# Kernel optimization log

Hardware: AMD Instinct MI355X
Metric: run time of the kernel (lower is better)

## Reference

```python
import jax, jax.numpy as jnp
import numpy as np

B, T, C = 4, 2048, 1024
N_HEAD = 16
HEAD_DIM = C // N_HEAD

def setup_inputs() -> dict:
    key = jax.random.key(0)
    k1, k2, k3, k4, k5 = jax.random.split(key, 5)
    sigma = (1.0 / C) ** 0.5  # encoder_var=1 default
    return {
        "x": jax.random.normal(k1, (B, T, C), dtype=jnp.float32),
        "W_attn": jax.random.normal(k2, (3 * C, C), dtype=jnp.float32) * sigma,
        "b_attn": jax.random.normal(k3, (3 * C,), dtype=jnp.float32),
        "W_proj": jax.random.normal(k4, (C, C), dtype=jnp.float32) * sigma,
        "b_proj": jax.random.normal(k5, (C,), dtype=jnp.float32),
    }

def reference(x, W_attn, b_attn, W_proj, b_proj):
    Bq, Tq, Cq = x.shape
    qkv = x @ W_attn.T + b_attn              # [B,T,3C]
    q, k, v = jnp.split(qkv, 3, axis=-1)
    def to_heads(t):
        return t.reshape(Bq, Tq, N_HEAD, HEAD_DIM).transpose(0, 2, 1, 3)  # [B,H,T,D]
    q, k, v = to_heads(q), to_heads(k), to_heads(v)
    # NOTE: original scales by 1/head_dim (not 1/sqrt(head_dim))
    att = jnp.einsum('bhqd,bhkd->bhqk', q, k) * (1.0 / HEAD_DIM)
    causal = jnp.tril(jnp.ones((Tq, Tq), dtype=bool))
    att = jnp.where(causal[None, None], att, -jnp.inf)
    att = jax.nn.softmax(att, axis=-1)
    y = jnp.einsum('bhqk,bhkd->bhqd', att, v)
    y = y.transpose(0, 2, 1, 3).reshape(Bq, Tq, Cq)
    return y @ W_proj.T + b_proj
```

## Files before the change

### kernel.cpp

```cpp
#include <hip/hip_runtime.h>

typedef __attribute__((ext_vector_type(8))) short s16x8;
typedef __attribute__((ext_vector_type(4))) float f32x4;
typedef __attribute__((ext_vector_type(4))) unsigned short u16x4;

#define T_  2048
#define C_  1024
#define D_  64

__device__ __forceinline__ unsigned short f2bf(float f){
  union { float fv; unsigned int u; } v; v.fv = f;
  unsigned int r = v.u + 0x7FFFu + ((v.u >> 16) & 1u);
  return (unsigned short)(r >> 16);
}

__device__ __forceinline__ float exp2_asm(float x){
  float r; asm("v_exp_f32 %0, %1" : "=v"(r) : "v"(x)); return r;
}
__device__ __forceinline__ unsigned int cvtpk(float lo, float hi){
  unsigned int r; asm("v_cvt_pk_bf16_f32 %0, %1, %2" : "=v"(r) : "v"(lo), "v"(hi)); return r;
}

__device__ __forceinline__ void gload_lds16(const void* g, void* l){
  __builtin_amdgcn_global_load_lds(
      (const __attribute__((address_space(1))) unsigned int*)g,
      (__attribute__((address_space(3))) unsigned int*)l, 16, 0, 0);
}

__global__ __launch_bounds__(256) void cvt_kernel(const float* __restrict__ src,
                                                  unsigned short* __restrict__ dst){
  size_t i = ((size_t)blockIdx.x * 256u + threadIdx.x) * 8u;
  f32x4 a = *(const f32x4*)(src + i);
  f32x4 b = *(const f32x4*)(src + i + 4);
  s16x8 o;
  #pragma unroll
  for (int j = 0; j < 4; ++j){ o[j] = (short)f2bf(a[j]); o[4+j] = (short)f2bf(b[j]); }
  *(s16x8*)(dst + i) = o;
}

template<int MODE>
__global__ __launch_bounds__(256) void gemm_bt(
    const unsigned short* __restrict__ A, const unsigned short* __restrict__ Bw,
    const float* __restrict__ bias, int M, int N, int K,
    unsigned short* __restrict__ q_ws, unsigned short* __restrict__ k_ws,
    unsigned short* __restrict__ vT_ws, float* __restrict__ out)
{
  __shared__ unsigned short As[2][128*32];
  __shared__ unsigned short Bs[2][128*32];
  const int tid = threadIdx.x;
  const int lane = tid & 63, wid = tid >> 6;
  const int g = lane >> 4, lr = lane & 15;
  const int m0 = blockIdx.y * 128, n0 = blockIdx.x * 128;
  const int wr = wid >> 1, wc = wid & 1;

  f32x4 acc[4][4];
  #pragma unroll
  for (int i = 0; i < 4; ++i)
    #pragma unroll
    for (int j = 0; j < 4; ++j) acc[i][j] = (f32x4){0.f,0.f,0.f,0.f};

  auto stage = [&](int kt, int buf){
    const int k0 = kt << 5;
    #pragma unroll
    for (int j = 0; j < 2; ++j){
      const int c = wid*128 + j*64 + lane;
      const int row = c >> 2, kc = c & 3;
      gload_lds16((const char*)A  + (((size_t)(m0+row))*K + k0)*2 + kc*16,
                  (char*)&As[buf][0] + (size_t)c*16);
      gload_lds16((const char*)Bw + (((size_t)(n0+row))*K + k0)*2 + kc*16,
                  (char*)&Bs[buf][0] + (size_t)c*16);
    }
  };

  const int nk = K >> 5;
  stage(0, 0);
  __syncthreads();

  for (int kt = 0; kt < nk; ++kt){
    const int cur = kt & 1;
    if (kt + 1 < nk) stage(kt + 1, cur ^ 1);
    s16x8 af[4], bf[4];
    #pragma unroll
    for (int i = 0; i < 4; ++i)
      af[i] = *(const s16x8*)&As[cur][(wr*64 + i*16 + lr)*32 + g*8];
    #pragma unroll
    for (int j = 0; j < 4; ++j)
      bf[j] = *(const s16x8*)&Bs[cur][(wc*64 + j*16 + lr)*32 + g*8];
    #pragma unroll
    for (int i = 0; i < 4; ++i)
      #pragma unroll
      for (int j = 0; j < 4; ++j)
        acc[i][j] = __builtin_amdgcn_mfma_f32_16x16x32_bf16(af[i], bf[j], acc[i][j], 0, 0, 0);
    __syncthreads();
  }

  #pragma unroll
  for (int i = 0; i < 4; ++i){
    #pragma unroll
    for (int j = 0; j < 4; ++j){
      const int n = n0 + wc*64 + j*16 + lr;
      const float bv = bias[n];
      #pragma unroll
      for (int r = 0; r < 4; ++r){
        const int m = m0 + wr*64 + i*16 + g*4 + r;
        const float val = acc[i][j][r] + bv;
        if (MODE == 0){
          const int which = n >> 10;
          const int cc = n & 1023;
          const int h = cc >> 6, d = cc & 63;
          const int bq = m >> 11, t = m & 2047;
          const int bh = bq*16 + h;
          if (which == 0)      q_ws[((size_t)bh*T_ + t)*D_ + d] = f2bf(val * 0.022542110013890054f);
          else if (which == 1) k_ws[((size_t)bh*T_ + t)*D_ + d] = f2bf(val);
          else                 vT_ws[((size_t)bh*D_ + d)*T_ + t] = f2bf(val);
        } else {
          out[(size_t)m*N + n] = val;
        }
      }
    }
  }
}

__global__ __launch_bounds__(256, 4) void attn_kernel(
    const unsigned short* __restrict__ q_ws, const unsigned short* __restrict__ k_ws,
    const unsigned short* __restrict__ vT_ws, unsigned short* __restrict__ y_ws)
{
  __shared__ __align__(16) unsigned short Ks[2][64*64];
  __shared__ __align__(16) unsigned short Vs[2][64*64];

  const int tid = threadIdx.x;
  const int lane = tid & 63, wid = tid >> 6;
  const int g = lane >> 4, lr = lane & 15;
  const int orig = (int)blockIdx.x;
  const int wgid = (orig & 7) * 128 + (orig >> 3);
  const int p  = wgid & 15;
  const int bh = wgid >> 4;
  const int qwA = p*64 + wid*16,  qwB = (31 - p)*64 + wid*16;
  const int qrowA = qwA + lr,     qrowB = qwB + lr;
  const int swz = (lr & 7) << 4;

  const unsigned short* Qb = q_ws  + (size_t)bh*T_*D_;
  const unsigned short* Kb = k_ws  + (size_t)bh*T_*D_;
  const unsigned short* Vb = vT_ws + (size_t)bh*D_*T_;

  auto stage = [&](int t, int buf){
    const int kt0 = t << 6;
    #pragma unroll
    for (int s = 0; s < 2; ++s){
      const int c = s*256 + tid;
      const int r = c >> 3;
      const int scol = ((c & 7) << 4) ^ ((r & 7) << 4);
      gload_lds16((const char*)Kb + ((size_t)(kt0 + r)*D_)*2 + scol,
                  (char*)&Ks[buf][0] + c*16);
      gload_lds16((const char*)Vb + ((size_t)r*T_ + kt0)*2 + scol,
                  (char*)&Vs[buf][0] + c*16);
    }
  };

  const s16x8 bqA0 = *(const s16x8*)&Qb[(size_t)(qwA+lr)*D_ + g*8];
  const s16x8 bqA1 = *(const s16x8*)&Qb[(size_t)(qwA+lr)*D_ + 32 + g*8];
  const s16x8 bqB0 = *(const s16x8*)&Qb[(size_t)(qwB+lr)*D_ + g*8];
  const s16x8 bqB1 = *(const s16x8*)&Qb[(size_t)(qwB+lr)*D_ + 32 + g*8];

  s16x8 ones;
  #pragma unroll
  for (int j = 0; j < 8; ++j) ones[j] = (short)0x3F80;

  f32x4 yA[4], yB[4];
  #pragma unroll
  for (int dt = 0; dt < 4; ++dt){ yA[dt] = (f32x4){0.f,0.f,0.f,0.f}; yB[dt] = (f32x4){0.f,0.f,0.f,0.f}; }
  f32x4 lacA = (f32x4){0.f,0.f,0.f,0.f}, lacB = (f32x4){0.f,0.f,0.f,0.f};
  float mA = -1e30f, mB = -1e30f;

  const int ntA = p + 1, ntB = 32 - p;
  stage(0, 0);
  __syncthreads();

  for (int t = 0; t < ntB; ++t){
    const int cur = t & 1;
    if (t + 1 < ntB) stage(t + 1, cur ^ 1);
    const int kt0 = t << 6;
    const unsigned short* Kt = &Ks[cur][0];
    const unsigned short* Vt = &Vs[cur][0];
    unsigned short* Pw = &Ks[cur][wid*1024];
    const bool actA = (t < ntA);

    f32x4 sB[4], sA[4];
    #pragma unroll
    for (int kk = 0; kk < 4; ++kk){
      const int row = kk*16 + lr;
      const s16x8 a0 = *(const s16x8*)&Kt[row*64 + (((g*16)      ^ swz) >> 1)];
      const s16x8 a1 = *(const s16x8*)&Kt[row*64 + (((64 + g*16) ^ swz) >> 1)];
      f32x4 acc = (f32x4){0.f,0.f,0.f,0.f};
      acc = __builtin_amdgcn_mfma_f32_16x16x32_bf16(a0, bqB0, acc, 0, 0, 0);
      acc = __builtin_amdgcn_mfma_f32_16x16x32_bf16(a1, bqB1, acc, 0, 0, 0);
      sB[kk] = acc;
      if (actA){
        f32x4 acc2 = (f32x4){0.f,0.f,0.f,0.f};
        acc2 = __builtin_amdgcn_mfma_f32_16x16x32_bf16(a0, bqA0, acc2, 0, 0, 0);
        acc2 = __builtin_amdgcn_mfma_f32_16x16x32_bf16(a1, bqA1, acc2, 0, 0, 0);
        sA[kk] = acc2;
      }
    }

    if (kt0 + 63 > qwB){
      #pragma unroll
      for (int kk = 0; kk < 4; ++kk)
        #pragma unroll
        for (int r = 0; r < 4; ++r)
          if (kt0 + kk*16 + g*4 + r > qrowB) sB[kk][r] = -1e30f;
    }
    {
      float m01 = fmaxf(fmaxf(sB[0][0], sB[0][1]), fmaxf(sB[0][2], sB[0][3]));
      float m23 = fmaxf(fmaxf(sB[1][0], sB[1][1]), fmaxf(sB[1][2], sB[1][3]));
      float m45 = fmaxf(fmaxf(sB[2][0], sB[2][1]), fmaxf(sB[2][2], sB[2][3]));
      float m67 = fmaxf(fmaxf(sB[3][0], sB[3][1]), fmaxf(sB[3][2], sB[3][3]));
      float mx = fmaxf(fmaxf(m01, m23), fmaxf(m45, m67));
      mx = fmaxf(mx, __shfl_xor(mx, 16, 64));
      mx = fmaxf(mx, __shfl_xor(mx, 32, 64));
      if (!__all(mx <= mB + 8.f)){
        const float mnew = fmaxf(mB, mx);
        const float corr = exp2_asm(mB - mnew);
        mB = mnew;
        lacB[0] *= corr;
        #pragma unroll
        for (int dt = 0; dt < 4; ++dt)
          #pragma unroll
          for (int r = 0; r < 4; ++r) yB[dt][r] *= corr;
      }
    }
    union { unsigned int u[2]; u16x4 v; } pkB[4];
    #pragma unroll
    for (int kk = 0; kk < 4; ++kk){
      const float e0 = exp2_asm(sB[kk][0] - mB);
      const float e1 = exp2_asm(sB[kk][1] - mB);
      const float e2 = exp2_asm(sB[kk][2] - mB);
      const float e3 = exp2_asm(sB[kk][3] - mB);
      pkB[kk].u[0] = cvtpk(e0, e1);
      pkB[kk].u[1] = cvtpk(e2, e3);
    }

    asm volatile("s_barrier" ::: "memory");

    #pragma unroll
    for (int kk = 0; kk < 4; ++kk)
      *(u16x4*)&Pw[lr*64 + (((kk*32 + g*8) ^ swz) >> 1)] = pkB[kk].v;
    asm volatile("" ::: "memory");
    {
      const s16x8 p0 = *(const s16x8*)&Pw[lr*64 + (((g*16)      ^ swz) >> 1)];
      const s16x8 p1 = *(const s16x8*)&Pw[lr*64 + (((64 + g*16) ^ swz) >> 1)];
      lacB = __builtin_amdgcn_mfma_f32_16x16x32_bf16(ones, p0, lacB, 0, 0, 0);
      lacB = __builtin_amdgcn_mfma_f32_16x16x32_bf16(ones, p1, lacB, 0, 0, 0);
      #pragma unroll
      for (int dt = 0; dt < 4; ++dt){
        const int vrow = dt*16 + lr;
        const s16x8 v0 = *(const s16x8*)&Vt[vrow*64 + (((g*16)      ^ swz) >> 1)];
        const s16x8 v1 = *(const s16x8*)&Vt[vrow*64 + (((64 + g*16) ^ swz) >> 1)];
        yB[dt] = __builtin_amdgcn_mfma_f32_16x16x32_bf16(v0, p0, yB[dt], 0, 0, 0);
        yB[dt] = __builtin_amdgcn_mfma_f32_16x16x32_bf16(v1, p1, yB[dt], 0, 0, 0);
      }
    }

    if (actA){
      if (kt0 + 63 > qwA){
        #pragma unroll
        for (int kk = 0; kk < 4; ++kk)
          #pragma unroll
          for (int r = 0; r < 4; ++r)
            if (kt0 + kk*16 + g*4 + r > qrowA) sA[kk][r] = -1e30f;
      }
      float m01 = fmaxf(fmaxf(sA[0][0], sA[0][1]), fmaxf(sA[0][2], sA[0][3]));
      float m23 = fmaxf(fmaxf(sA[1][0], sA[1][1]), fmaxf(sA[1][2], sA[1][3]));
      float m45 = fmaxf(fmaxf(sA[2][0], sA[2][1]), fmaxf(sA[2][2], sA[2][3]));
      float m67 = fmaxf(fmaxf(sA[3][0], sA[3][1]), fmaxf(sA[3][2], sA[3][3]));
      float mx = fmaxf(fmaxf(m01, m23), fmaxf(m45, m67));
      mx = fmaxf(mx, __shfl_xor(mx, 16, 64));
      mx = fmaxf(mx, __shfl_xor(mx, 32, 64));
      if (!__all(mx <= mA + 8.f)){
        const float mnew = fmaxf(mA, mx);
        const float corr = exp2_asm(mA - mnew);
        mA = mnew;
        lacA[0] *= corr;
        #pragma unroll
        for (int dt = 0; dt < 4; ++dt)
          #pragma unroll
          for (int r = 0; r < 4; ++r) yA[dt][r] *= corr;
      }
      union { unsigned int u[2]; u16x4 v; } pkA[4];
      #pragma unroll
      for (int kk = 0; kk < 4; ++kk){
        const float e0 = exp2_asm(sA[kk][0] - mA);
        const float e1 = exp2_asm(sA[kk][1] - mA);
        const float e2 = exp2_asm(sA[kk][2] - mA);
        const float e3 = exp2_asm(sA[kk][3] - mA);
        pkA[kk].u[0] = cvtpk(e0, e1);
        pkA[kk].u[1] = cvtpk(e2, e3);
      }
      asm volatile("" ::: "memory");
      #pragma unroll
      for (int kk = 0; kk < 4; ++kk)
        *(u16x4*)&Pw[lr*64 + (((kk*32 + g*8) ^ swz) >> 1)] = pkA[kk].v;
      asm volatile("" ::: "memory");
      const s16x8 p0 = *(const s16x8*)&Pw[lr*64 + (((g*16)      ^ swz) >> 1)];
      const s16x8 p1 = *(const s16x8*)&Pw[lr*64 + (((64 + g*16) ^ swz) >> 1)];
      lacA = __builtin_amdgcn_mfma_f32_16x16x32_bf16(ones, p0, lacA, 0, 0, 0);
      lacA = __builtin_amdgcn_mfma_f32_16x16x32_bf16(ones, p1, lacA, 0, 0, 0);
      #pragma unroll
      for (int dt = 0; dt < 4; ++dt){
        const int vrow = dt*16 + lr;
        const s16x8 v0 = *(const s16x8*)&Vt[vrow*64 + (((g*16)      ^ swz) >> 1)];
        const s16x8 v1 = *(const s16x8*)&Vt[vrow*64 + (((64 + g*16) ^ swz) >> 1)];
        yA[dt] = __builtin_amdgcn_mfma_f32_16x16x32_bf16(v0, p0, yA[dt], 0, 0, 0);
        yA[dt] = __builtin_amdgcn_mfma_f32_16x16x32_bf16(v1, p1, yA[dt], 0, 0, 0);
      }
    }

    __syncthreads();
  }

  const int bq = bh >> 4, h = bh & 15;
  {
    const float inv = 1.f / lacB[0];
    #pragma unroll
    for (int dt = 0; dt < 4; ++dt){
      union { unsigned int u[2]; u16x4 v; } w;
      w.u[0] = cvtpk(yB[dt][0]*inv, yB[dt][1]*inv);
      w.u[1] = cvtpk(yB[dt][2]*inv, yB[dt][3]*inv);
      *(u16x4*)&y_ws[((size_t)(bq*T_ + qwB + lr))*C_ + h*64 + dt*16 + g*4] = w.v;
    }
  }
  {
    const float inv = 1.f / lacA[0];
    #pragma unroll
    for (int dt = 0; dt < 4; ++dt){
      union { unsigned int u[2]; u16x4 v; } w;
      w.u[0] = cvtpk(yA[dt][0]*inv, yA[dt][1]*inv);
      w.u[1] = cvtpk(yA[dt][2]*inv, yA[dt][3]*inv);
      *(u16x4*)&y_ws[((size_t)(bq*T_ + qwA + lr))*C_ + h*64 + dt*16 + g*4] = w.v;
    }
  }
}

extern "C" void kernel_launch(void* const* d_in, const int* in_sizes, int n_in,
                              void* d_out, int out_size, void* d_ws, size_t ws_size,
                              hipStream_t stream) {
  const float* x  = (const float*)d_in[0];
  const float* Wa = (const float*)d_in[1];
  const float* ba = (const float*)d_in[2];
  const float* Wp = (const float*)d_in[3];
  const float* bp = (const float*)d_in[4];
  float* out = (float*)d_out;

  char* ws = (char*)d_ws;
  const size_t MB = 1024u*1024u;
  unsigned short* xb  = (unsigned short*)(ws + 0);
  unsigned short* wab = (unsigned short*)(ws + 16*MB);
  unsigned short* wpb = (unsigned short*)(ws + 22*MB);
  unsigned short* qws = (unsigned short*)(ws + 24*MB);
  unsigned short* kws = (unsigned short*)(ws + 40*MB);
  unsigned short* vT  = (unsigned short*)(ws + 56*MB);
  unsigned short* yws = (unsigned short*)(ws + 72*MB);

  cvt_kernel<<<4096, 256, 0, stream>>>(x,  xb);
  cvt_kernel<<<1536, 256, 0, stream>>>(Wa, wab);
  cvt_kernel<<< 512, 256, 0, stream>>>(Wp, wpb);

  gemm_bt<0><<<dim3(24, 64), 256, 0, stream>>>(xb, wab, ba, 8192, 3072, 1024,
                                               qws, kws, vT, nullptr);
  attn_kernel<<<dim3(1024), 256, 0, stream>>>(qws, kws, vT, yws);
  gemm_bt<1><<<dim3(8, 64), 256, 0, stream>>>(yws, wpb, bp, 8192, 1024, 1024,
                                              nullptr, nullptr, nullptr, out);
}
```

Measured before the change: 207.7 us.

## Retile GEMMs to 256x128x64 with swizzled LDS, deeper prefetch and XCD remap

The projection GEMM kernel moves to 512-thread blocks computing 256x128 tiles with a K-step of 64. It uses XOR-swizzled LDS layouts to avoid bank conflicts and keeps two stages in flight via vmcnt-based waits instead of full syncthreads. Block IDs are remapped across the 8 XCDs for L2 locality, and MFMA sections run at raised priority. The aim is more operand reuse per LDS load and better overlap of global loads with compute. The cost is higher LDS use (96KB per block) and register pressure, which reduce occupancy.

```diff
diff --git a/kernel.cpp b/kernel.cpp
--- a/kernel.cpp
+++ b/kernel.cpp
@@ -39,71 +39,123 @@
 }
 
 template<int MODE>
-__global__ __launch_bounds__(256) void gemm_bt(
+__global__ __launch_bounds__(512, 2) void gemm_bt(
     const unsigned short* __restrict__ A, const unsigned short* __restrict__ Bw,
-    const float* __restrict__ bias, int M, int N, int K,
+    const float* __restrict__ bias, int M, int N, int K, int nbx,
     unsigned short* __restrict__ q_ws, unsigned short* __restrict__ k_ws,
     unsigned short* __restrict__ vT_ws, float* __restrict__ out)
 {
-  __shared__ unsigned short As[2][128*32];
-  __shared__ unsigned short Bs[2][128*32];
+  __shared__ unsigned short Asm[2][256*64];
+  __shared__ unsigned short Bsm[2][128*64];
   const int tid = threadIdx.x;
   const int lane = tid & 63, wid = tid >> 6;
   const int g = lane >> 4, lr = lane & 15;
-  const int m0 = blockIdx.y * 128, n0 = blockIdx.x * 128;
-  const int wr = wid >> 1, wc = wid & 1;
-
-  f32x4 acc[4][4];
+  const int wm = wid >> 2, wn = wid & 3;
+  const int nwg = (int)gridDim.x;
+  const int cpx = nwg >> 3;
+  const int orig = (int)blockIdx.x;
+  const int wgid = (orig & 7) * cpx + (orig >> 3);
+  const int bx = wgid % nbx, by = wgid / nbx;
+  const int m0 = by * 256, n0 = bx * 128;
+  const int swz = (lr & 7) << 4;
+
+  f32x4 acc[8][2];
   #pragma unroll
-  for (int i = 0; i < 4; ++i)
-    #pragma unroll
-    for (int j = 0; j < 4; ++j) acc[i][j] = (f32x4){0.f,0.f,0.f,0.f};
+  for (int i = 0; i < 8; ++i){ acc[i][0] = (f32x4){0.f,0.f,0.f,0.f}; acc[i][1] = (f32x4){0.f,0.f,0.f,0.f}; }
 
   auto stage = [&](int kt, int buf){
-    const int k0 = kt << 5;
+    const int k0 = kt << 6;
+    #pragma unroll
+    for (int j = 0; j < 4; ++j){
+      const int c = j*512 + tid;
+      const int row = c >> 3, jc = (c & 7) << 4;
+      gload_lds16((const char*)A + ((size_t)(m0+row)*K + k0)*2 + (jc ^ ((row & 7) << 4)),
+                  (char*)&Asm[buf][0] + (size_t)c*16);
+    }
     #pragma unroll
     for (int j = 0; j < 2; ++j){
-      const int c = wid*128 + j*64 + lane;
-      const int row = c >> 2, kc = c & 3;
-      gload_lds16((const char*)A  + (((size_t)(m0+row))*K + k0)*2 + kc*16,
-                  (char*)&As[buf][0] + (size_t)c*16);
-      gload_lds16((const char*)Bw + (((size_t)(n0+row))*K + k0)*2 + kc*16,
-                  (char*)&Bs[buf][0] + (size_t)c*16);
+      const int c = j*512 + tid;
+      const int row = c >> 3, jc = (c & 7) << 4;
+      gload_lds16((const char*)Bw + ((size_t)(n0+row)*K + k0)*2 + (jc ^ ((row & 7) << 4)),
+                  (char*)&Bsm[buf][0] + (size_t)c*16);
     }
   };
 
-  const int nk = K >> 5;
+  const int nk = K >> 6;
   stage(0, 0);
-  __syncthreads();
+  stage(1, 1);
 
   for (int kt = 0; kt < nk; ++kt){
     const int cur = kt & 1;
-    if (kt + 1 < nk) stage(kt + 1, cur ^ 1);
-    s16x8 af[4], bf[4];
-    #pragma unroll
-    for (int i = 0; i < 4; ++i)
-      af[i] = *(const s16x8*)&As[cur][(wr*64 + i*16 + lr)*32 + g*8];
-    #pragma unroll
-    for (int j = 0; j < 4; ++j)
-      bf[j] = *(const s16x8*)&Bs[cur][(wc*64 + j*16 + lr)*32 + g*8];
-    #pragma unroll
-    for (int i = 0; i < 4; ++i)
-      #pragma unroll
-      for (int j = 0; j < 4; ++j)
-        acc[i][j] = __builtin_amdgcn_mfma_f32_16x16x32_bf16(af[i], bf[j], acc[i][j], 0, 0, 0);
-    __syncthreads();
+    if (kt < nk - 1) asm volatile("s_waitcnt vmcnt(6)" ::: "memory");
+    else             asm volatile("s_waitcnt vmcnt(0)" ::: "memory");
+    asm volatile("s_barrier" ::: "memory");
+
+    const char* At = (const char*)&Asm[cur][0];
+    const char* Bt = (const char*)&Bsm[cur][0];
+
+    s16x8 bf[2][2];
+    #pragma unroll
+    for (int ni = 0; ni < 2; ++ni){
+      const int row = wn*32 + ni*16 + lr;
+      #pragma unroll
+      for (int s = 0; s < 2; ++s)
+        bf[ni][s] = *(const s16x8*)(Bt + row*128 + ((s*64 + g*16) ^ swz));
+    }
+
+    {
+      s16x8 af[4][2];
+      #pragma unroll
+      for (int mi = 0; mi < 4; ++mi){
+        const int row = wm*128 + mi*16 + lr;
+        #pragma unroll
+        for (int s = 0; s < 2; ++s)
+          af[mi][s] = *(const s16x8*)(At + row*128 + ((s*64 + g*16) ^ swz));
+      }
+      __builtin_amdgcn_s_setprio(1);
+      #pragma unroll
+      for (int mi = 0; mi < 4; ++mi)
+        #pragma unroll
+        for (int ni = 0; ni < 2; ++ni){
+          acc[mi][ni] = __builtin_amdgcn_mfma_f32_16x16x32_bf16(af[mi][0], bf[ni][0], acc[mi][ni], 0, 0, 0);
+          acc[mi][ni] = __builtin_amdgcn_mfma_f32_16x16x32_bf16(af[mi][1], bf[ni][1], acc[mi][ni], 0, 0, 0);
+        }
+      __builtin_amdgcn_s_setprio(0);
+    }
+    {
+      s16x8 af[4][2];
+      #pragma unroll
+      for (int mi = 0; mi < 4; ++mi){
+        const int row = wm*128 + (mi+4)*16 + lr;
+        #pragma unroll
+        for (int s = 0; s < 2; ++s)
+          af[mi][s] = *(const s16x8*)(At + row*128 + ((s*64 + g*16) ^ swz));
+      }
+      __builtin_amdgcn_s_setprio(1);
+      #pragma unroll
+      for (int mi = 0; mi < 4; ++mi)
+        #pragma unroll
+        for (int ni = 0; ni < 2; ++ni){
+          acc[mi+4][ni] = __builtin_amdgcn_mfma_f32_16x16x32_bf16(af[mi][0], bf[ni][0], acc[mi+4][ni], 0, 0, 0);
+          acc[mi+4][ni] = __builtin_amdgcn_mfma_f32_16x16x32_bf16(af[mi][1], bf[ni][1], acc[mi+4][ni], 0, 0, 0);
+        }
+      __builtin_amdgcn_s_setprio(0);
+    }
+
+    asm volatile("s_barrier" ::: "memory");
+    if (kt + 2 < nk) stage(kt + 2, cur);
   }
 
   #pragma unroll
-  for (int i = 0; i < 4; ++i){
-    #pragma unroll
-    for (int j = 0; j < 4; ++j){
-      const int n = n0 + wc*64 + j*16 + lr;
+  for (int mi = 0; mi < 8; ++mi){
+    #pragma unroll
+    for (int ni = 0; ni < 2; ++ni){
+      const int n = n0 + wn*32 + ni*16 + lr;
       const float bv = bias[n];
       #pragma unroll
       for (int r = 0; r < 4; ++r){
-        const int m = m0 + wr*64 + i*16 + g*4 + r;
-        const float val = acc[i][j][r] + bv;
+        const int m = m0 + wm*128 + mi*16 + g*4 + r;
+        const float val = acc[mi][ni][r] + bv;
         if (MODE == 0){
           const int which = n >> 10;
           const int cc = n & 1023;
@@ -365,9 +417,9 @@
   cvt_kernel<<<1536, 256, 0, stream>>>(Wa, wab);
   cvt_kernel<<< 512, 256, 0, stream>>>(Wp, wpb);
 
-  gemm_bt<0><<<dim3(24, 64), 256, 0, stream>>>(xb, wab, ba, 8192, 3072, 1024,
-                                               qws, kws, vT, nullptr);
+  gemm_bt<0><<<dim3(768), 512, 0, stream>>>(xb, wab, ba, 8192, 3072, 1024, 24,
+                                            qws, kws, vT, nullptr);
   attn_kernel<<<dim3(1024), 256, 0, stream>>>(qws, kws, vT, yws);
-  gemm_bt<1><<<dim3(8, 64), 256, 0, stream>>>(yws, wpb, bp, 8192, 1024, 1024,
-                                              nullptr, nullptr, nullptr, out);
-}
+  gemm_bt<1><<<dim3(256), 512, 0, stream>>>(yws, wpb, bp, 8192, 1024, 1024, 8,
+                                            nullptr, nullptr, nullptr, out);
+}
```

New measurement: 204.3 us. Within noise of the previous version (-1.6%).

## Restructure GEMM with BK=64, XOR-swizzled LDS, vmcnt pipelining and XCD-aware block remap

Applied to the files above, without the earlier changes.

The GEMM kernels now load 64-wide K tiles into an XOR-swizzled LDS layout to avoid bank conflicts. Two stages are kept in flight, waited on with explicit vmcnt counts and raw barriers instead of __syncthreads. Blocks are remapped across the eight XCDs for better L2 locality, and MFMA sections get raised wave priority. The cost is twice the LDS (64KB per block) and a hand-written wait/barrier protocol that must stay correct.

```diff
diff --git a/kernel.cpp b/kernel.cpp
--- a/kernel.cpp
+++ b/kernel.cpp
@@ -39,19 +39,25 @@
 }
 
 template<int MODE>
-__global__ __launch_bounds__(256) void gemm_bt(
+__global__ __launch_bounds__(256, 2) void gemm_bt(
     const unsigned short* __restrict__ A, const unsigned short* __restrict__ Bw,
-    const float* __restrict__ bias, int M, int N, int K,
+    const float* __restrict__ bias, int M, int N, int K, int nbx,
     unsigned short* __restrict__ q_ws, unsigned short* __restrict__ k_ws,
     unsigned short* __restrict__ vT_ws, float* __restrict__ out)
 {
-  __shared__ unsigned short As[2][128*32];
-  __shared__ unsigned short Bs[2][128*32];
+  __shared__ unsigned short Asm[2][128*64];
+  __shared__ unsigned short Bsm[2][128*64];
   const int tid = threadIdx.x;
   const int lane = tid & 63, wid = tid >> 6;
   const int g = lane >> 4, lr = lane & 15;
-  const int m0 = blockIdx.y * 128, n0 = blockIdx.x * 128;
   const int wr = wid >> 1, wc = wid & 1;
+  const int nwg = (int)gridDim.x;
+  const int cpx = nwg >> 3;
+  const int orig = (int)blockIdx.x;
+  const int wgid = (orig & 7) * cpx + (orig >> 3);
+  const int bx = wgid % nbx, by = wgid / nbx;
+  const int m0 = by * 128, n0 = bx * 128;
+  const int swz = (lr & 7) << 4;
 
   f32x4 acc[4][4];
   #pragma unroll
@@ -60,50 +66,68 @@
     for (int j = 0; j < 4; ++j) acc[i][j] = (f32x4){0.f,0.f,0.f,0.f};
 
   auto stage = [&](int kt, int buf){
-    const int k0 = kt << 5;
-    #pragma unroll
-    for (int j = 0; j < 2; ++j){
-      const int c = wid*128 + j*64 + lane;
-      const int row = c >> 2, kc = c & 3;
-      gload_lds16((const char*)A  + (((size_t)(m0+row))*K + k0)*2 + kc*16,
-                  (char*)&As[buf][0] + (size_t)c*16);
-      gload_lds16((const char*)Bw + (((size_t)(n0+row))*K + k0)*2 + kc*16,
-                  (char*)&Bs[buf][0] + (size_t)c*16);
+    const int k0 = kt << 6;
+    #pragma unroll
+    for (int j = 0; j < 4; ++j){
+      const int c = j*256 + tid;
+      const int row = c >> 3, jc = c & 7;
+      const int sc = (jc ^ (row & 7)) << 4;
+      gload_lds16((const char*)A  + ((size_t)(m0+row)*K + k0)*2 + sc,
+                  (char*)&Asm[buf][0] + (size_t)c*16);
+      gload_lds16((const char*)Bw + ((size_t)(n0+row)*K + k0)*2 + sc,
+                  (char*)&Bsm[buf][0] + (size_t)c*16);
     }
   };
 
-  const int nk = K >> 5;
+  const int nk = K >> 6;
   stage(0, 0);
-  __syncthreads();
-
-  for (int kt = 0; kt < nk; ++kt){
-    const int cur = kt & 1;
-    if (kt + 1 < nk) stage(kt + 1, cur ^ 1);
-    s16x8 af[4], bf[4];
-    #pragma unroll
-    for (int i = 0; i < 4; ++i)
-      af[i] = *(const s16x8*)&As[cur][(wr*64 + i*16 + lr)*32 + g*8];
-    #pragma unroll
-    for (int j = 0; j < 4; ++j)
-      bf[j] = *(const s16x8*)&Bs[cur][(wc*64 + j*16 + lr)*32 + g*8];
-    #pragma unroll
-    for (int i = 0; i < 4; ++i)
-      #pragma unroll
-      for (int j = 0; j < 4; ++j)
-        acc[i][j] = __builtin_amdgcn_mfma_f32_16x16x32_bf16(af[i], bf[j], acc[i][j], 0, 0, 0);
-    __syncthreads();
-  }
-
-  #pragma unroll
-  for (int i = 0; i < 4; ++i){
-    #pragma unroll
-    for (int j = 0; j < 4; ++j){
-      const int n = n0 + wc*64 + j*16 + lr;
+  stage(1, 1);
+
+  for (int t = 0; t < nk; ++t){
+    const int cur = t & 1;
+    if (t < nk - 1) asm volatile("s_waitcnt vmcnt(8)" ::: "memory");
+    else            asm volatile("s_waitcnt vmcnt(0)" ::: "memory");
+    asm volatile("s_barrier" ::: "memory");
+
+    const char* At = (const char*)&Asm[cur][0];
+    const char* Bt = (const char*)&Bsm[cur][0];
+
+    #pragma unroll
+    for (int s = 0; s < 2; ++s){
+      s16x8 af[4], bf[4];
+      #pragma unroll
+      for (int mi = 0; mi < 4; ++mi){
+        const int row = wr*64 + mi*16 + lr;
+        af[mi] = *(const s16x8*)(At + row*128 + ((s*64 + g*16) ^ swz));
+      }
+      #pragma unroll
+      for (int ni = 0; ni < 4; ++ni){
+        const int row = wc*64 + ni*16 + lr;
+        bf[ni] = *(const s16x8*)(Bt + row*128 + ((s*64 + g*16) ^ swz));
+      }
+      __builtin_amdgcn_s_setprio(1);
+      #pragma unroll
+      for (int mi = 0; mi < 4; ++mi)
+        #pragma unroll
+        for (int ni = 0; ni < 4; ++ni)
+          acc[mi][ni] = __builtin_amdgcn_mfma_f32_16x16x32_bf16(af[mi], bf[ni], acc[mi][ni], 0, 0, 0);
+      __builtin_amdgcn_s_setprio(0);
+    }
+
+    asm volatile("s_barrier" ::: "memory");
+    if (t + 2 < nk) stage(t + 2, cur);
+  }
+
+  #pragma unroll
+  for (int mi = 0; mi < 4; ++mi){
+    #pragma unroll
+    for (int ni = 0; ni < 4; ++ni){
+      const int n = n0 + wc*64 + ni*16 + lr;
       const float bv = bias[n];
       #pragma unroll
       for (int r = 0; r < 4; ++r){
-        const int m = m0 + wr*64 + i*16 + g*4 + r;
-        const float val = acc[i][j][r] + bv;
+        const int m = m0 + wr*64 + mi*16 + g*4 + r;
+        const float val = acc[mi][ni][r] + bv;
         if (MODE == 0){
           const int which = n >> 10;
           const int cc = n & 1023;
@@ -365,9 +389,9 @@
   cvt_kernel<<<1536, 256, 0, stream>>>(Wa, wab);
   cvt_kernel<<< 512, 256, 0, stream>>>(Wp, wpb);
 
-  gemm_bt<0><<<dim3(24, 64), 256, 0, stream>>>(xb, wab, ba, 8192, 3072, 1024,
-                                               qws, kws, vT, nullptr);
+  gemm_bt<0><<<dim3(1536), 256, 0, stream>>>(xb, wab, ba, 8192, 3072, 1024, 24,
+                                             qws, kws, vT, nullptr);
   attn_kernel<<<dim3(1024), 256, 0, stream>>>(qws, kws, vT, yws);
-  gemm_bt<1><<<dim3(8, 64), 256, 0, stream>>>(yws, wpb, bp, 8192, 1024, 1024,
-                                              nullptr, nullptr, nullptr, out);
-}
+  gemm_bt<1><<<dim3(512), 256, 0, stream>>>(yws, wpb, bp, 8192, 1024, 1024, 8,
+                                            nullptr, nullptr, nullptr, out);
+}
```

New measurement: 195.0 us. 6.1% less time.
